# Performance work log

Measured on AMD Instinct MI355X. Metric: run time of the kernel, lower is better.

Reference implementation:

```python
import jax, jax.numpy as jnp
import numpy as np

N, G, E, H, Z = 50000, 2000, 800000, 512, 64
BN_EPS = 1e-5


def setup_inputs() -> dict:
    key = jax.random.key(0)
    ks = jax.random.split(key, 10)
    x = jax.random.normal(ks[0], (N, G), dtype=jnp.float32)
    edge_index = jax.random.randint(ks[1], (2, E), 0, N, dtype=jnp.int32)
    s1 = 1.0 / np.sqrt(G)
    s2 = 1.0 / np.sqrt(H)
    return {
        "x": x,
        "edge_index": edge_index,
        "W1l": jax.random.normal(ks[2], (G, H), dtype=jnp.float32) * s1,
        "b1": jnp.zeros((H,), jnp.float32),
        "W1r": jax.random.normal(ks[3], (G, H), dtype=jnp.float32) * s1,
        "bn_gamma": jax.random.uniform(ks[4], (H,), dtype=jnp.float32) + 0.5,
        "bn_beta": jax.random.normal(ks[5], (H,), dtype=jnp.float32) * 0.1,
        "bn_mean": jax.random.normal(ks[6], (H,), dtype=jnp.float32) * 0.1,
        "bn_var": jax.random.uniform(ks[7], (H,), dtype=jnp.float32) + 0.5,
        "W2l": jax.random.normal(ks[8], (H, Z), dtype=jnp.float32) * s2,
        "b2": jnp.zeros((Z,), jnp.float32),
        "W2r": jax.random.normal(ks[9], (H, Z), dtype=jnp.float32) * s2,
    }


def _sage_conv(h, src, dst, Wl, bl, Wr, n_nodes):
    # mean aggregation of source features at destination nodes
    msg = h[src]  # [E, D] gather
    agg = jax.ops.segment_sum(msg, dst, num_segments=n_nodes)
    cnt = jax.ops.segment_sum(jnp.ones((src.shape[0],), h.dtype), dst, num_segments=n_nodes)
    agg = agg / jnp.maximum(cnt, 1.0)[:, None]
    # PyG SAGEConv: lin_l(agg) + lin_r(x), bias only on lin_l
    return agg @ Wl + bl + h @ Wr


def reference(x, edge_index, W1l, b1, W1r, bn_gamma, bn_beta, bn_mean, bn_var, W2l, b2, W2r):
    src, dst = edge_index[0], edge_index[1]
    n = x.shape[0]
    h = _sage_conv(x, src, dst, W1l, b1, W1r, n)  # [N, H]
    # BatchNorm1d (eval mode: running stats) + ReLU; dropout is identity at inference
    h = (h - bn_mean) * (bn_gamma / jnp.sqrt(bn_var + BN_EPS)) + bn_beta
    h = jax.nn.relu(h)
    z = _sage_conv(h, src, dst, W2l, b2, W2r, n)  # [N, Z]
    return z
```

## Files before the change

kernel.cpp:

```cpp
#include <hip/hip_runtime.h>


#define BN_EPS 1e-5f
#define GK 2000
#define KP 2048
#define NT1C 63
#define NT1P 64
#define NT2 16

typedef __attribute__((ext_vector_type(8))) short bf16x8;
typedef __attribute__((ext_vector_type(4))) float f32x4;
typedef unsigned short u16x8 __attribute__((ext_vector_type(8)));

__device__ inline unsigned short f2bf(float f) {
    union { float f; unsigned u; } v; v.f = f;
    unsigned r = (v.u + 0x7fffu + ((v.u >> 16) & 1u)) >> 16;
    return (unsigned short)r;
}
__device__ inline float bf2f(unsigned short u) {
    union { unsigned u; float f; } v; v.u = ((unsigned)u) << 16;
    return v.f;
}

#define GLL16(gp, lp) __builtin_amdgcn_global_load_lds( \
    (const __attribute__((address_space(1))) void*)(gp), \
    (__attribute__((address_space(3))) void*)(lp), 16, 0, 0)

__global__ void count_kernel(const int* __restrict__ ei, int E, int* __restrict__ cnt) {
    int i = blockIdx.x * blockDim.x + threadIdx.x;
    if (i < E) atomicAdd(&cnt[ei[E + i]], 1);
}

__global__ __launch_bounds__(1024) void scan_kernel(const int* __restrict__ cnt,
                                                    int* __restrict__ row_start, int n) {
    __shared__ int part[1024];
    int t = threadIdx.x;
    int chunk = (n + 1023) >> 10;
    int lo = t * chunk;
    int hi = lo + chunk; if (hi > n) hi = n;
    int s = 0;
    for (int i = lo; i < hi; ++i) s += cnt[i];
    part[t] = s;
    __syncthreads();
    for (int off = 1; off < 1024; off <<= 1) {
        int add = (t >= off) ? part[t - off] : 0;
        __syncthreads();
        part[t] += add;
        __syncthreads();
    }
    int run = (t == 0) ? 0 : part[t - 1];
    for (int i = lo; i < hi; ++i) { row_start[i] = run; run += cnt[i]; }
    if (t == 1023) row_start[n] = part[1023];
}

__global__ void fill_kernel(const int* __restrict__ ei, int E,
                            const int* __restrict__ row_start,
                            int* __restrict__ cursor, int* __restrict__ colidx) {
    int i = blockIdx.x * blockDim.x + threadIdx.x;
    if (i < E) {
        int d = ei[E + i];
        int p = atomicAdd(&cursor[d], 1);
        colidx[row_start[d] + p] = ei[i];
    }
}

__global__ __launch_bounds__(256) void conv_kernel(const float* __restrict__ x,
                                                   unsigned short* __restrict__ xb) {
    int row = blockIdx.x;
    int k8 = threadIdx.x;
    unsigned short us[8];
    if (k8 < 250) {
        const float4* p = (const float4*)(x + (size_t)row * 2000 + k8 * 8);
        float4 v0 = p[0], v1 = p[1];
        us[0]=f2bf(v0.x); us[1]=f2bf(v0.y); us[2]=f2bf(v0.z); us[3]=f2bf(v0.w);
        us[4]=f2bf(v1.x); us[5]=f2bf(v1.y); us[6]=f2bf(v1.z); us[7]=f2bf(v1.w);
    } else {
#pragma unroll
        for (int j = 0; j < 8; ++j) us[j] = 0;
    }
    *(u16x8*)&xb[(size_t)row * 2048 + k8 * 8] = *(u16x8*)us;
}

__global__ __launch_bounds__(256) void prep_bt(const float* __restrict__ W1l,
                                               const float* __restrict__ W1r,
                                               unsigned short* __restrict__ BT) {
    int idx = blockIdx.x * 256 + threadIdx.x;
    int c  = idx >> 8;
    int k0 = (idx & 255) << 3;
    const float* W = (c < 512) ? (W1l + c) : (W1r + (c - 512));
    unsigned short us[8];
#pragma unroll
    for (int j = 0; j < 8; ++j) {
        int k = k0 + j;
        float v = (k < GK) ? W[(size_t)k * 512] : 0.0f;
        us[j] = f2bf(v);
    }
    *(u16x8*)&BT[(size_t)c * KP + k0] = *(u16x8*)us;
}

__global__ __launch_bounds__(256) void prep_bt2(const float* __restrict__ W2l,
                                                const float* __restrict__ W2r,
                                                unsigned short* __restrict__ BT2) {
    int idx = blockIdx.x * 256 + threadIdx.x;
    int c  = idx >> 6;
    int k0 = (idx & 63) << 3;
    const float* W = (c < 64) ? (W2l + c) : (W2r + (c - 64));
    unsigned short us[8];
#pragma unroll
    for (int j = 0; j < 8; ++j) us[j] = f2bf(W[(size_t)(k0 + j) * 64]);
    *(u16x8*)&BT2[(size_t)c * 512 + k0] = *(u16x8*)us;
}

__global__ __launch_bounds__(256) void gemm1_pure(
    const unsigned short* __restrict__ xb, int M,
    const unsigned short* __restrict__ BT,
    unsigned short* __restrict__ Y)
{
    __shared__ __align__(16) unsigned short As[3][4096];
    __shared__ __align__(16) unsigned short Bs[3][4096];

    const int t = threadIdx.x, wid = t >> 6, lane = t & 63;
    const int nby = (M + 127) >> 7;
    const int b   = blockIdx.x;
    const int swz = (b & 7) * nby + (b >> 3);
    const int row0 = (swz >> 3) << 7;
    const int col0 = (swz & 7) << 7;

    const int c0 = wid * 64 + lane, c1 = c0 + 256;
    const int g0 = ((c0 & 3) ^ ((c0 >> 2) & 3)) << 3;
    const int g1 = ((c1 & 3) ^ ((c1 >> 2) & 3)) << 3;
    int ra0 = row0 + (c0 >> 2); if (ra0 >= M) ra0 = M - 1;
    int ra1 = row0 + (c1 >> 2); if (ra1 >= M) ra1 = M - 1;
    const unsigned short* aS0 = xb + (size_t)ra0 * KP + g0;
    const unsigned short* aS1 = xb + (size_t)ra1 * KP + g1;
    const unsigned short* bS0 = BT + (size_t)(col0 + (c0 >> 2)) * KP + g0;
    const unsigned short* bS1 = BT + (size_t)(col0 + (c1 >> 2)) * KP + g1;

    const int wr = wid >> 1, wc = wid & 1;
    const int fr16 = lane & 15;
    const int gswr = ((lane >> 4) ^ (fr16 & 3)) << 4;

    f32x4 acc[4][4];
#pragma unroll
    for (int m = 0; m < 4; ++m)
#pragma unroll
        for (int n = 0; n < 4; ++n) acc[m][n] = (f32x4)0.0f;

#define STG1(kt, buf) do {                                             \
        unsigned short* ab_ = &As[buf][0];                             \
        unsigned short* bb_ = &Bs[buf][0];                             \
        GLL16(aS0 + (size_t)(kt) * 32, ab_ + (wid * 64) * 8);          \
        GLL16(aS1 + (size_t)(kt) * 32, ab_ + (256 + wid * 64) * 8);    \
        GLL16(bS0 + (size_t)(kt) * 32, bb_ + (wid * 64) * 8);          \
        GLL16(bS1 + (size_t)(kt) * 32, bb_ + (256 + wid * 64) * 8);    \
    } while (0)

    STG1(0, 0);
    STG1(1, 1);

    int rb = 0;
    for (int it = 0; it < NT1P; ++it) {
        if (it == NT1P - 1) {
            asm volatile("s_waitcnt vmcnt(0)" ::: "memory");
        } else {
            asm volatile("s_waitcnt vmcnt(4)" ::: "memory");
        }
        __builtin_amdgcn_s_barrier();
        __builtin_amdgcn_sched_barrier(0);

        const char* Ab = (const char*)&As[rb][0];
        const char* Bb = (const char*)&Bs[rb][0];
        bf16x8 af[4], bfr[4];
#pragma unroll
        for (int m = 0; m < 4; ++m)
            af[m] = *(const bf16x8*)(Ab + ((wr * 64 + m * 16 + fr16) << 6) + gswr);
#pragma unroll
        for (int n = 0; n < 4; ++n)
            bfr[n] = *(const bf16x8*)(Bb + ((wc * 64 + n * 16 + fr16) << 6) + gswr);

        if (it + 2 < NT1P) {
            int wb = rb + 2; if (wb >= 3) wb -= 3;
            STG1(it + 2, wb);
        }

        __builtin_amdgcn_s_setprio(1);
#pragma unroll
        for (int m = 0; m < 4; ++m)
#pragma unroll
            for (int n = 0; n < 4; ++n)
                acc[m][n] = __builtin_amdgcn_mfma_f32_16x16x32_bf16(
                    af[m], bfr[n], acc[m][n], 0, 0, 0);
        __builtin_amdgcn_s_setprio(0);

        rb = (rb == 2) ? 0 : rb + 1;
    }
#undef STG1

    const int crow = (lane >> 4) << 2;
#pragma unroll
    for (int m = 0; m < 4; ++m) {
        int rbase = row0 + wr * 64 + m * 16 + crow;
#pragma unroll
        for (int r = 0; r < 4; ++r) {
            int row = rbase + r;
            if (row < M) {
                unsigned short* Yp = Y + (size_t)row * 1024 + col0 + wc * 64 + fr16;
#pragma unroll
                for (int n = 0; n < 4; ++n)
                    Yp[n * 16] = f2bf(acc[m][n][r]);
            }
        }
    }
}

__global__ __launch_bounds__(256) void gemm1_cvt(
    const float* __restrict__ A, int M,
    const unsigned short* __restrict__ BT,
    unsigned short* __restrict__ Y)
{
    __shared__ __align__(16) unsigned short As[128][32];
    __shared__ __align__(16) unsigned short Bs[2][128][32];

    const int t    = threadIdx.x;
    const int wid  = t >> 6;
    const int lane = t & 63;
    const int nby = (M + 127) >> 7;
    const int b   = blockIdx.x;
    const int swz = (b & 7) * nby + (b >> 3);
    const int row0 = (swz >> 3) << 7;
    const int col0 = (swz & 7) << 7;

    const int ar  = t >> 1;
    const int akq = (t & 1) << 4;
    int garow = row0 + ar; if (garow >= M) garow = M - 1;
    const float* aptr = A + (size_t)garow * GK + akq;

    const int i0 = wid * 64 + lane;
    const unsigned short* bptr0 = BT + ((size_t)(col0 + (i0 >> 2)) * KP + ((i0 & 3) << 3));
    const unsigned short* bptr1 = bptr0 + (size_t)64 * KP;

    const int wr   = wid >> 1, wc = wid & 1;
    const int fr16 = lane & 15;
    const int kb8  = (lane >> 4) << 3;

    f32x4 acc[4][4];
#pragma unroll
    for (int m = 0; m < 4; ++m)
#pragma unroll
        for (int n = 0; n < 4; ++n) acc[m][n] = (f32x4)0.0f;

    GLL16(bptr0, &Bs[0][wid * 16][0]);
    GLL16(bptr1, &Bs[0][64 + wid * 16][0]);

    float frg[16];
    {
        const float4* p = (const float4*)aptr;
        float4 v0 = p[0], v1 = p[1], v2 = p[2], v3 = p[3];
        frg[0]=v0.x; frg[1]=v0.y; frg[2]=v0.z;  frg[3]=v0.w;
        frg[4]=v1.x; frg[5]=v1.y; frg[6]=v1.z;  frg[7]=v1.w;
        frg[8]=v2.x; frg[9]=v2.y; frg[10]=v2.z; frg[11]=v2.w;
        frg[12]=v3.x;frg[13]=v3.y;frg[14]=v3.z; frg[15]=v3.w;
    }

    int cur = 0;
    for (int it = 0; it < NT1C; ++it) {
        {
            unsigned short us[16];
#pragma unroll
            for (int j = 0; j < 16; ++j) us[j] = f2bf(frg[j]);
            *(u16x8*)&As[ar][akq]     = *(u16x8*)&us[0];
            *(u16x8*)&As[ar][akq + 8] = *(u16x8*)&us[8];
        }
        __syncthreads();

        if (it + 1 < NT1C) {
            int kb = (it + 1) * 32 + akq;
            if (kb < GK) {
                const float4* p = (const float4*)(aptr + (size_t)(it + 1) * 32);
                float4 v0 = p[0], v1 = p[1], v2 = p[2], v3 = p[3];
                frg[0]=v0.x; frg[1]=v0.y; frg[2]=v0.z;  frg[3]=v0.w;
                frg[4]=v1.x; frg[5]=v1.y; frg[6]=v1.z;  frg[7]=v1.w;
                frg[8]=v2.x; frg[9]=v2.y; frg[10]=v2.z; frg[11]=v2.w;
                frg[12]=v3.x;frg[13]=v3.y;frg[14]=v3.z; frg[15]=v3.w;
            } else {
#pragma unroll
                for (int j = 0; j < 16; ++j) frg[j] = 0.0f;
            }
            const unsigned short* bp = bptr0 + (size_t)(it + 1) * 32;
            GLL16(bp,                   &Bs[cur ^ 1][wid * 16][0]);
            GLL16(bp + (size_t)64 * KP, &Bs[cur ^ 1][64 + wid * 16][0]);
        }

        bf16x8 af[4], bfr[4];
#pragma unroll
        for (int m = 0; m < 4; ++m)
            af[m] = *(const bf16x8*)&As[wr * 64 + m * 16 + fr16][kb8];
#pragma unroll
        for (int n = 0; n < 4; ++n)
            bfr[n] = *(const bf16x8*)&Bs[cur][wc * 64 + n * 16 + fr16][kb8];
#pragma unroll
        for (int m = 0; m < 4; ++m)
#pragma unroll
            for (int n = 0; n < 4; ++n)
                acc[m][n] = __builtin_amdgcn_mfma_f32_16x16x32_bf16(
                    af[m], bfr[n], acc[m][n], 0, 0, 0);

        __syncthreads();
        cur ^= 1;
    }

    const int crow = (lane >> 4) << 2;
#pragma unroll
    for (int m = 0; m < 4; ++m) {
        int rbase = row0 + wr * 64 + m * 16 + crow;
#pragma unroll
        for (int r = 0; r < 4; ++r) {
            int row = rbase + r;
            if (row < M) {
                unsigned short* Yp = Y + (size_t)row * 1024 + col0 + wc * 64 + fr16;
#pragma unroll
                for (int n = 0; n < 4; ++n)
                    Yp[n * 16] = f2bf(acc[m][n][r]);
            }
        }
    }
}

__global__ __launch_bounds__(256) void agg1_kernel(
    const unsigned short* __restrict__ Y, unsigned short* __restrict__ Hh,
    const int* __restrict__ row_start, const int* __restrict__ colidx,
    const float* __restrict__ b1, const float* __restrict__ gamma,
    const float* __restrict__ beta, const float* __restrict__ mean,
    const float* __restrict__ var, int n)
{
    int wid  = (blockIdx.x * blockDim.x + threadIdx.x) >> 6;
    int lane = threadIdx.x & 63;
    if (wid >= n) return;
    int c0 = lane * 8;
    float sc[8], sh[8], bb[8];
#pragma unroll
    for (int j = 0; j < 8; ++j) {
        int c = c0 + j;
        sc[j] = gamma[c] * rsqrtf(var[c] + BN_EPS);
        sh[j] = beta[c] - mean[c] * sc[j];
        bb[j] = b1[c];
    }
    int s0 = row_start[wid], s1 = row_start[wid + 1];
    float acc[8] = {0, 0, 0, 0, 0, 0, 0, 0};
    for (int i = s0; i < s1; ++i) {
        int src = colidx[i];
        u16x8 v = *(const u16x8*)&Y[(size_t)src * 1024 + c0];
#pragma unroll
        for (int j = 0; j < 8; ++j) acc[j] += bf2f(v[j]);
    }
    float inv = 1.0f / fmaxf((float)(s1 - s0), 1.0f);
    u16x8 sv = *(const u16x8*)&Y[(size_t)wid * 1024 + 512 + c0];
    unsigned short o[8];
#pragma unroll
    for (int j = 0; j < 8; ++j) {
        float pre = acc[j] * inv + bb[j] + bf2f(sv[j]);
        float h = pre * sc[j] + sh[j];
        o[j] = f2bf(fmaxf(h, 0.0f));
    }
    *(u16x8*)&Hh[(size_t)wid * 512 + c0] = *(u16x8*)o;
}

__global__ __launch_bounds__(256) void gemm2_bf16(
    const unsigned short* __restrict__ Hh, int M,
    const unsigned short* __restrict__ BT2,
    unsigned short* __restrict__ U)
{
    __shared__ __align__(16) unsigned short As[2][128][32];
    __shared__ __align__(16) unsigned short Bs[2][128][32];

    const int t    = threadIdx.x;
    const int wid  = t >> 6;
    const int lane = t & 63;
    const int row0 = blockIdx.x << 7;

    const int c_lo = wid * 64 + lane;
    const int c_hi = c_lo + 256;
    int ra = row0 + (c_lo >> 2); if (ra >= M) ra = M - 1;
    int rb = row0 + (c_hi >> 2); if (rb >= M) rb = M - 1;
    const unsigned short* aSrc0 = Hh + (size_t)ra * 512 + ((c_lo & 3) << 3);
    const unsigned short* aSrc1 = Hh + (size_t)rb * 512 + ((c_hi & 3) << 3);
    const unsigned short* bSrc0 = BT2 + (size_t)(c_lo >> 2) * 512 + ((c_lo & 3) << 3);
    const unsigned short* bSrc1 = BT2 + (size_t)(c_hi >> 2) * 512 + ((c_hi & 3) << 3);

    const int wr   = wid >> 1, wc = wid & 1;
    const int fr16 = lane & 15;
    const int kb8  = (lane >> 4) << 3;

    f32x4 acc[4][4];
#pragma unroll
    for (int m = 0; m < 4; ++m)
#pragma unroll
        for (int n = 0; n < 4; ++n) acc[m][n] = (f32x4)0.0f;

#define STAGE2(kt, buf) do {                                                  \
        int ko = (kt) * 32;                                                   \
        GLL16(aSrc0 + ko, (unsigned short*)&As[buf][0][0] + (size_t)(wid * 64) * 8);        \
        GLL16(aSrc1 + ko, (unsigned short*)&As[buf][0][0] + (size_t)(256 + wid * 64) * 8);  \
        GLL16(bSrc0 + ko, (unsigned short*)&Bs[buf][0][0] + (size_t)(wid * 64) * 8);        \
        GLL16(bSrc1 + ko, (unsigned short*)&Bs[buf][0][0] + (size_t)(256 + wid * 64) * 8);  \
    } while (0)

    STAGE2(0, 0);
    int cur = 0;
    for (int it = 0; it < NT2; ++it) {
        __syncthreads();
        if (it + 1 < NT2) STAGE2(it + 1, cur ^ 1);

        bf16x8 af[4], bfr[4];
#pragma unroll
        for (int m = 0; m < 4; ++m)
            af[m] = *(const bf16x8*)&As[cur][wr * 64 + m * 16 + fr16][kb8];
#pragma unroll
        for (int n = 0; n < 4; ++n)
            bfr[n] = *(const bf16x8*)&Bs[cur][wc * 64 + n * 16 + fr16][kb8];
#pragma unroll
        for (int m = 0; m < 4; ++m)
#pragma unroll
            for (int n = 0; n < 4; ++n)
                acc[m][n] = __builtin_amdgcn_mfma_f32_16x16x32_bf16(
                    af[m], bfr[n], acc[m][n], 0, 0, 0);
        cur ^= 1;
    }
#undef STAGE2

    const int crow = (lane >> 4) << 2;
#pragma unroll
    for (int m = 0; m < 4; ++m) {
        int rbase = row0 + wr * 64 + m * 16 + crow;
#pragma unroll
        for (int r = 0; r < 4; ++r) {
            int row = rbase + r;
            if (row < M) {
                unsigned short* Up = U + (size_t)row * 128 + wc * 64 + fr16;
#pragma unroll
                for (int n = 0; n < 4; ++n)
                    Up[n * 16] = f2bf(acc[m][n][r]);
            }
        }
    }
}

__global__ __launch_bounds__(256) void agg2_kernel(
    const unsigned short* __restrict__ U,
    const int* __restrict__ row_start, const int* __restrict__ colidx,
    const float* __restrict__ b2, float* __restrict__ out, int n)
{
    int wid  = (blockIdx.x * blockDim.x + threadIdx.x) >> 6;
    int lane = threadIdx.x & 63;
    if (wid >= n) return;
    int s0 = row_start[wid], s1 = row_start[wid + 1];
    float acc = 0.f;
    for (int i = s0; i < s1; ++i) {
        int src = colidx[i];
        acc += bf2f(U[(size_t)src * 128 + lane]);
    }
    float inv = 1.0f / fmaxf((float)(s1 - s0), 1.0f);
    float z = acc * inv + b2[lane] + bf2f(U[(size_t)wid * 128 + 64 + lane]);
    out[(size_t)wid * 64 + lane] = z;
}

extern "C" void kernel_launch(void* const* d_in, const int* in_sizes, int n_in,
                              void* d_out, int out_size, void* d_ws, size_t ws_size,
                              hipStream_t stream) {
    const float* x     = (const float*)d_in[0];
    const int*   ei    = (const int*)d_in[1];
    const float* W1l   = (const float*)d_in[2];
    const float* b1    = (const float*)d_in[3];
    const float* W1r   = (const float*)d_in[4];
    const float* gamma = (const float*)d_in[5];
    const float* beta  = (const float*)d_in[6];
    const float* mean  = (const float*)d_in[7];
    const float* var   = (const float*)d_in[8];
    const float* W2l   = (const float*)d_in[9];
    const float* b2    = (const float*)d_in[10];
    const float* W2r   = (const float*)d_in[11];
    float* out = (float*)d_out;

    const int N = in_sizes[0] / 2000;
    const int E = in_sizes[1] / 2;
    const int nby = (N + 127) / 128;

    char* ws = (char*)d_ws;

    size_t need = (size_t)N * KP * 2 + (size_t)N * 1024 * 2
                + (size_t)1024 * KP * 2 + (size_t)128 * 512 * 2
                + ((size_t)3 * N + 8 + (size_t)E) * 4;

    if (ws_size >= need) {
        unsigned short* xb  = (unsigned short*)ws;
        unsigned short* Y   = xb + (size_t)N * KP;
        unsigned short* BT  = Y + (size_t)N * 1024;
        unsigned short* BT2 = BT + (size_t)1024 * KP;
        int* cnt       = (int*)(BT2 + (size_t)128 * 512);
        int* row_start = cnt + N;
        int* cursor    = row_start + N + 4;
        int* colidx    = cursor + N;
        unsigned short* Hh = xb;
        unsigned short* U  = Y;

        hipMemsetAsync(cnt, 0, (size_t)N * sizeof(int), stream);
        hipMemsetAsync(cursor, 0, (size_t)N * sizeof(int), stream);

        prep_bt<<<1024, 256, 0, stream>>>(W1l, W1r, BT);
        prep_bt2<<<32, 256, 0, stream>>>(W2l, W2r, BT2);
        conv_kernel<<<N, 256, 0, stream>>>(x, xb);

        int eb = (E + 255) / 256;
        count_kernel<<<eb, 256, 0, stream>>>(ei, E, cnt);
        scan_kernel<<<1, 1024, 0, stream>>>(cnt, row_start, N);
        fill_kernel<<<eb, 256, 0, stream>>>(ei, E, row_start, cursor, colidx);

        gemm1_pure<<<8 * nby, 256, 0, stream>>>(xb, N, BT, Y);
        agg1_kernel<<<(N + 3) / 4, 256, 0, stream>>>(
            Y, Hh, row_start, colidx, b1, gamma, beta, mean, var, N);
        gemm2_bf16<<<nby, 256, 0, stream>>>(Hh, N, BT2, U);
        agg2_kernel<<<(N + 3) / 4, 256, 0, stream>>>(
            U, row_start, colidx, b2, out, N);
    } else {
        unsigned short* Y   = (unsigned short*)ws;
        unsigned short* Hh  = Y + (size_t)N * 1024;
        unsigned short* U   = Hh + (size_t)N * 512;
        unsigned short* BT  = U + (size_t)N * 128;
        unsigned short* BT2 = BT + (size_t)1024 * KP;
        int* cnt       = (int*)(BT2 + (size_t)128 * 512);
        int* row_start = cnt + N;
        int* cursor    = row_start + N + 4;
        int* colidx    = cursor + N;

        hipMemsetAsync(cnt, 0, (size_t)N * sizeof(int), stream);
        hipMemsetAsync(cursor, 0, (size_t)N * sizeof(int), stream);

        prep_bt<<<1024, 256, 0, stream>>>(W1l, W1r, BT);
        prep_bt2<<<32, 256, 0, stream>>>(W2l, W2r, BT2);

        int eb = (E + 255) / 256;
        count_kernel<<<eb, 256, 0, stream>>>(ei, E, cnt);
        scan_kernel<<<1, 1024, 0, stream>>>(cnt, row_start, N);
        fill_kernel<<<eb, 256, 0, stream>>>(ei, E, row_start, cursor, colidx);

        gemm1_cvt<<<8 * nby, 256, 0, stream>>>(x, N, BT, Y);
        agg1_kernel<<<(N + 3) / 4, 256, 0, stream>>>(
            Y, Hh, row_start, colidx, b1, gamma, beta, mean, var, N);
        gemm2_bf16<<<nby, 256, 0, stream>>>(Hh, N, BT2, U);
        agg2_kernel<<<(N + 3) / 4, 256, 0, stream>>>(
            U, row_start, colidx, b2, out, N);
    }
}
```

Before: 779.0 us.

## Enlarge layer-1 GEMM tile to 256x256 with 8 waves; reuse count array as cursor

The pure-bf16 layer-1 GEMM now uses 256x256 output tiles computed by 512 threads (8 waves, each holding a 128x64 accumulator block), doubling LDS staging buffers. The larger tile raises arithmetic intensity and cuts redundant A/B global loads across blocks. In exchange it raises register pressure (32 accumulator tiles per wave) and LDS use, lowering occupancy and leaving fewer workgroups to fill the GPU. Separately, the CSR fill kernel decrements the per-node count array instead of incrementing a separate cursor, removing one memset and one N-sized buffer.

New measurement: 771.1 us. Within noise of the previous version (-1.0%).

```diff
diff --git a/kernel.cpp b/kernel.cpp
--- a/kernel.cpp
+++ b/kernel.cpp
@@ -55,11 +55,11 @@
 
 __global__ void fill_kernel(const int* __restrict__ ei, int E,
                             const int* __restrict__ row_start,
-                            int* __restrict__ cursor, int* __restrict__ colidx) {
+                            int* __restrict__ cnt, int* __restrict__ colidx) {
     int i = blockIdx.x * blockDim.x + threadIdx.x;
     if (i < E) {
         int d = ei[E + i];
-        int p = atomicAdd(&cursor[d], 1);
+        int p = atomicSub(&cnt[d], 1) - 1;
         colidx[row_start[d] + p] = ei[i];
     }
 }
@@ -111,22 +111,25 @@
     *(u16x8*)&BT2[(size_t)c * 512 + k0] = *(u16x8*)us;
 }
 
-__global__ __launch_bounds__(256) void gemm1_pure(
+__global__ __launch_bounds__(512) void gemm1_256(
     const unsigned short* __restrict__ xb, int M,
     const unsigned short* __restrict__ BT,
     unsigned short* __restrict__ Y)
 {
-    __shared__ __align__(16) unsigned short As[3][4096];
-    __shared__ __align__(16) unsigned short Bs[3][4096];
+    __shared__ __align__(16) unsigned short As[3][8192];
+    __shared__ __align__(16) unsigned short Bs[3][8192];
 
     const int t = threadIdx.x, wid = t >> 6, lane = t & 63;
-    const int nby = (M + 127) >> 7;
+    const int nbr = (M + 255) >> 8;
+    const int nwg = nbr * 4;
     const int b   = blockIdx.x;
-    const int swz = (b & 7) * nby + (b >> 3);
-    const int row0 = (swz >> 3) << 7;
-    const int col0 = (swz & 7) << 7;
-
-    const int c0 = wid * 64 + lane, c1 = c0 + 256;
+    int swz;
+    if ((nwg & 7) == 0) swz = (b & 7) * (nwg >> 3) + (b >> 3);
+    else swz = b;
+    const int row0 = (swz >> 2) << 8;
+    const int col0 = (swz & 3) << 8;
+
+    const int c0 = t, c1 = t + 512;
     const int g0 = ((c0 & 3) ^ ((c0 >> 2) & 3)) << 3;
     const int g1 = ((c1 & 3) ^ ((c1 >> 2) & 3)) << 3;
     int ra0 = row0 + (c0 >> 2); if (ra0 >= M) ra0 = M - 1;
@@ -136,27 +139,27 @@
     const unsigned short* bS0 = BT + (size_t)(col0 + (c0 >> 2)) * KP + g0;
     const unsigned short* bS1 = BT + (size_t)(col0 + (c1 >> 2)) * KP + g1;
 
-    const int wr = wid >> 1, wc = wid & 1;
+    const int wr = wid >> 2, wc = wid & 3;
     const int fr16 = lane & 15;
     const int gswr = ((lane >> 4) ^ (fr16 & 3)) << 4;
 
-    f32x4 acc[4][4];
-#pragma unroll
-    for (int m = 0; m < 4; ++m)
+    f32x4 acc[8][4];
+#pragma unroll
+    for (int m = 0; m < 8; ++m)
 #pragma unroll
         for (int n = 0; n < 4; ++n) acc[m][n] = (f32x4)0.0f;
 
-#define STG1(kt, buf) do {                                             \
-        unsigned short* ab_ = &As[buf][0];                             \
-        unsigned short* bb_ = &Bs[buf][0];                             \
-        GLL16(aS0 + (size_t)(kt) * 32, ab_ + (wid * 64) * 8);          \
-        GLL16(aS1 + (size_t)(kt) * 32, ab_ + (256 + wid * 64) * 8);    \
-        GLL16(bS0 + (size_t)(kt) * 32, bb_ + (wid * 64) * 8);          \
-        GLL16(bS1 + (size_t)(kt) * 32, bb_ + (256 + wid * 64) * 8);    \
+#define STG(kt, buf) do {                                          \
+        unsigned short* ab_ = &As[buf][0];                         \
+        unsigned short* bb_ = &Bs[buf][0];                         \
+        GLL16(aS0 + (size_t)(kt) * 32, ab_ + c0 * 8);              \
+        GLL16(aS1 + (size_t)(kt) * 32, ab_ + c1 * 8);              \
+        GLL16(bS0 + (size_t)(kt) * 32, bb_ + c0 * 8);              \
+        GLL16(bS1 + (size_t)(kt) * 32, bb_ + c1 * 8);              \
     } while (0)
 
-    STG1(0, 0);
-    STG1(1, 1);
+    STG(0, 0);
+    STG(1, 1);
 
     int rb = 0;
     for (int it = 0; it < NT1P; ++it) {
@@ -170,22 +173,22 @@
 
         const char* Ab = (const char*)&As[rb][0];
         const char* Bb = (const char*)&Bs[rb][0];
-        bf16x8 af[4], bfr[4];
-#pragma unroll
-        for (int m = 0; m < 4; ++m)
-            af[m] = *(const bf16x8*)(Ab + ((wr * 64 + m * 16 + fr16) << 6) + gswr);
+        bf16x8 af[8], bfr[4];
+#pragma unroll
+        for (int m = 0; m < 8; ++m)
+            af[m] = *(const bf16x8*)(Ab + ((wr * 128 + m * 16 + fr16) << 6) + gswr);
 #pragma unroll
         for (int n = 0; n < 4; ++n)
             bfr[n] = *(const bf16x8*)(Bb + ((wc * 64 + n * 16 + fr16) << 6) + gswr);
 
         if (it + 2 < NT1P) {
             int wb = rb + 2; if (wb >= 3) wb -= 3;
-            STG1(it + 2, wb);
+            STG(it + 2, wb);
         }
 
         __builtin_amdgcn_s_setprio(1);
 #pragma unroll
-        for (int m = 0; m < 4; ++m)
+        for (int m = 0; m < 8; ++m)
 #pragma unroll
             for (int n = 0; n < 4; ++n)
                 acc[m][n] = __builtin_amdgcn_mfma_f32_16x16x32_bf16(
@@ -194,12 +197,12 @@
 
         rb = (rb == 2) ? 0 : rb + 1;
     }
-#undef STG1
+#undef STG
 
     const int crow = (lane >> 4) << 2;
 #pragma unroll
-    for (int m = 0; m < 4; ++m) {
-        int rbase = row0 + wr * 64 + m * 16 + crow;
+    for (int m = 0; m < 8; ++m) {
+        int rbase = row0 + wr * 128 + m * 16 + crow;
 #pragma unroll
         for (int r = 0; r < 4; ++r) {
             int row = rbase + r;
@@ -489,7 +492,7 @@
 
     size_t need = (size_t)N * KP * 2 + (size_t)N * 1024 * 2
                 + (size_t)1024 * KP * 2 + (size_t)128 * 512 * 2
-                + ((size_t)3 * N + 8 + (size_t)E) * 4;
+                + ((size_t)2 * N + 8 + (size_t)E) * 4;
 
     if (ws_size >= need) {
         unsigned short* xb  = (unsigned short*)ws;
@@ -498,13 +501,11 @@
         unsigned short* BT2 = BT + (size_t)1024 * KP;
         int* cnt       = (int*)(BT2 + (size_t)128 * 512);
         int* row_start = cnt + N;
-        int* cursor    = row_start + N + 4;
-        int* colidx    = cursor + N;
+        int* colidx    = row_start + N + 4;
         unsigned short* Hh = xb;
         unsigned short* U  = Y;
 
         hipMemsetAsync(cnt, 0, (size_t)N * sizeof(int), stream);
-        hipMemsetAsync(cursor, 0, (size_t)N * sizeof(int), stream);
 
         prep_bt<<<1024, 256, 0, stream>>>(W1l, W1r, BT);
         prep_bt2<<<32, 256, 0, stream>>>(W2l, W2r, BT2);
@@ -513,9 +514,10 @@
         int eb = (E + 255) / 256;
         count_kernel<<<eb, 256, 0, stream>>>(ei, E, cnt);
         scan_kernel<<<1, 1024, 0, stream>>>(cnt, row_start, N);
-        fill_kernel<<<eb, 256, 0, stream>>>(ei, E, row_start, cursor, colidx);
-
-        gemm1_pure<<<8 * nby, 256, 0, stream>>>(xb, N, BT, Y);
+        fill_kernel<<<eb, 256, 0, stream>>>(ei, E, row_start, cnt, colidx);
+
+        int nbr = (N + 255) / 256;
+        gemm1_256<<<nbr * 4, 512, 0, stream>>>(xb, N, BT, Y);
         agg1_kernel<<<(N + 3) / 4, 256, 0, stream>>>(
             Y, Hh, row_start, colidx, b1, gamma, beta, mean, var, N);
         gemm2_bf16<<<nby, 256, 0, stream>>>(Hh, N, BT2, U);
@@ -529,11 +531,9 @@
         unsigned short* BT2 = BT + (size_t)1024 * KP;
         int* cnt       = (int*)(BT2 + (size_t)128 * 512);
         int* row_start = cnt + N;
-        int* cursor    = row_start + N + 4;
-        int* colidx    = cursor + N;
+        int* colidx    = row_start + N + 4;
 
         hipMemsetAsync(cnt, 0, (size_t)N * sizeof(int), stream);
-        hipMemsetAsync(cursor, 0, (size_t)N * sizeof(int), stream);
 
         prep_bt<<<1024, 256, 0, stream>>>(W1l, W1r, BT);
         prep_bt2<<<32, 256, 0, stream>>>(W2l, W2r, BT2);
@@ -541,7 +541,7 @@
         int eb = (E + 255) / 256;
         count_kernel<<<eb, 256, 0, stream>>>(ei, E, cnt);
         scan_kernel<<<1, 1024, 0, stream>>>(cnt, row_start, N);
-        fill_kernel<<<eb, 256, 0, stream>>>(ei, E, row_start, cursor, colidx);
+        fill_kernel<<<eb, 256, 0, stream>>>(ei, E, row_start, cnt, colidx);
 
         gemm1_cvt<<<8 * nby, 256, 0, stream>>>(x, N, BT, Y);
         agg1_kernel<<<(N + 3) / 4, 256, 0, stream>>>(
```
